# Performance work log

Hardware: AMD Instinct MI355X
Metric: run time of the kernel (lower is better)

## Reference

```python
import jax, jax.numpy as jnp
import numpy as np

B, D, N = 8, 1024, 1024
INTER, H = 512, 16
EPS = 1e-5


def conv1x1(x, W, b):
    # x: (B, Cin, N), W: (Cout, Cin), b: (Cout,) -> (B, Cout, N)
    return jnp.einsum('oc,bcn->bon', W, x) + b[None, :, None]


def setup_inputs() -> dict:
    key = jax.random.key(0)
    ks = jax.random.split(key, 12)
    s = 0.02
    v = jax.random.normal(ks[0], (B, D, N), jnp.float32)
    mask = (jax.random.uniform(ks[1], (B, N)) < 0.9).astype(jnp.float32)
    Wg = jax.random.normal(ks[2], (INTER, D), jnp.float32) * s
    bg = jax.random.normal(ks[3], (INTER,), jnp.float32) * s
    Wt = jax.random.normal(ks[4], (INTER, D), jnp.float32) * s
    bt = jax.random.normal(ks[5], (INTER,), jnp.float32) * s
    Wp = jax.random.normal(ks[6], (INTER, D), jnp.float32) * s
    bp = jax.random.normal(ks[7], (INTER,), jnp.float32) * s
    Ww = jax.random.normal(ks[8], (D, INTER), jnp.float32) * s
    bw = jax.random.normal(ks[9], (D,), jnp.float32) * s
    bn_gamma = jax.random.normal(ks[10], (D,), jnp.float32) * s + 1.0
    bn_beta = jax.random.normal(ks[11], (D,), jnp.float32) * s
    bn_mean = jnp.zeros((D,), jnp.float32)
    bn_var = jnp.ones((D,), jnp.float32)
    return {"v": v, "mask": mask, "Wg": Wg, "bg": bg, "Wt": Wt, "bt": bt,
            "Wp": Wp, "bp": bp, "Ww": Ww, "bw": bw, "bn_gamma": bn_gamma,
            "bn_beta": bn_beta, "bn_mean": bn_mean, "bn_var": bn_var}


def reference(v, mask, Wg, bg, Wt, bt, Wp, bp, Ww, bw,
              bn_gamma, bn_beta, bn_mean, bn_var):
    b, d, n = v.shape
    hd = INTER // H  # head dim
    # projections (1x1 conv == per-node linear); move to (B, N, INTER)
    g_v = conv1x1(v, Wg, bg).transpose(0, 2, 1) * mask[:, :, None]
    theta = conv1x1(v, Wt, bt).transpose(0, 2, 1)
    phi = conv1x1(v, Wp, bp).transpose(0, 2, 1)
    theta4 = theta.reshape(b, n, H, hd)  # (B, N, H, hd)
    phi4 = phi.reshape(b, n, H, hd)
    g4 = g_v.reshape(b, n, H, hd)
    # relation matrix R: (B, H, N, N)
    R = jnp.einsum('bnhd,bmhd->bhnm', theta4, phi4)
    C = jnp.sum(mask, axis=1)  # (B,)
    Rm = (R / C[:, None, None, None]) * mask[:, None, :, None] * mask[:, None, None, :]
    # aggregate: (B, N, H, hd)
    y = jnp.einsum('bhnm,bmhd->bnhd', Rm, g4).reshape(b, n, INTER)
    y = y.transpose(0, 2, 1)  # (B, INTER, N)
    # output projection + BatchNorm1d (eval form) + residual
    Wy = conv1x1(y, Ww, bw)
    inv = bn_gamma / jnp.sqrt(bn_var + EPS)
    Wy = (Wy - bn_mean[None, :, None]) * inv[None, :, None] + bn_beta[None, :, None]
    Wy = Wy * mask[:, None, :]
    return Wy + v
```

## Files before the change

### kernel.cpp

```cpp
#include <hip/hip_runtime.h>
#include <hip/hip_bf16.h>
#include <stdint.h>

#define B_ 8
#define D_ 1024
#define N_ 1024
#define INTER_ 512
#define H_ 16
#define EPS_ 1e-5f

typedef __attribute__((ext_vector_type(8))) short bf16x8;
typedef __attribute__((ext_vector_type(4))) float f32x4;
typedef __attribute__((ext_vector_type(4))) unsigned short u16x4;
typedef __attribute__((ext_vector_type(8))) unsigned short u16x8;

__device__ __forceinline__ unsigned short f2bf(float f) {
  union { float f; uint32_t u; } v; v.f = f;
  uint32_t r = (v.u + 0x7FFFu + ((v.u >> 16) & 1u)) >> 16;
  return (unsigned short)r;
}

__device__ __forceinline__ void gload_lds16(const void* g, void* l) {
  __builtin_amdgcn_global_load_lds(
      (const __attribute__((address_space(1))) void*)g,
      (__attribute__((address_space(3))) void*)l, 16, 0, 0);
}

__global__ __launch_bounds__(256) void k_prep(
    const float* __restrict__ v, const float* __restrict__ Wt,
    const float* __restrict__ Wp, const float* __restrict__ Wg,
    const float* __restrict__ Ww, const float* __restrict__ bt,
    const float* __restrict__ bp, const float* __restrict__ bg,
    const float* __restrict__ mask, unsigned short* __restrict__ vT,
    unsigned short* __restrict__ Wall, unsigned short* __restrict__ Wwb,
    float* __restrict__ ball, float* __restrict__ invC) {
  const int blk = blockIdx.x, tid = threadIdx.x;
  if (blk < 2048) {
    __shared__ short T[64 * 72];
    const int b = blk >> 8, tile = blk & 255;
    const int n0 = (tile & 15) * 64, d0 = (tile >> 4) * 64;
    const float* src = v + ((size_t)b * D_ + d0) * N_ + n0;
    const int c = tid & 15, rg = tid >> 4;
#pragma unroll
    for (int i = 0; i < 4; ++i) {
      const int r = rg * 4 + i;
      float4 f = *(const float4*)(src + (size_t)r * N_ + c * 4);
      const int nl = c * 4;
      T[(nl + 0) * 72 + r] = f2bf(f.x);
      T[(nl + 1) * 72 + r] = f2bf(f.y);
      T[(nl + 2) * 72 + r] = f2bf(f.z);
      T[(nl + 3) * 72 + r] = f2bf(f.w);
    }
    __syncthreads();
    unsigned short* dst = vT + ((size_t)b * N_ + n0) * D_ + d0;
    const int ch = tid & 7, nr = tid >> 3;
#pragma unroll
    for (int jj = 0; jj < 2; ++jj) {
      const int nl = nr + jj * 32;
      u16x8 val = *(const u16x8*)&T[nl * 72 + ch * 8];
      *(u16x8*)(dst + (size_t)nl * D_ + ch * 8) = val;
    }
  } else if (blk < 4096) {
    const int idx4 = (blk - 2048) * 256 + tid;
    const int total1 = 1536 * 1024 / 4;
    if (idx4 < total1) {
      const int idx = idx4 * 4;
      const int row = idx >> 10, c = idx & 1023;
      const float* src = row < 512    ? Wt + row * 1024 + c
                         : row < 1024 ? Wp + (row - 512) * 1024 + c
                                      : Wg + (row - 1024) * 1024 + c;
      float4 f = *(const float4*)src;
      u16x4 o = {f2bf(f.x), f2bf(f.y), f2bf(f.z), f2bf(f.w)};
      *(u16x4*)(Wall + idx) = o;
    } else {
      const int idx = (idx4 - total1) * 4;
      float4 f = *(const float4*)(Ww + idx);
      u16x4 o = {f2bf(f.x), f2bf(f.y), f2bf(f.z), f2bf(f.w)};
      *(u16x4*)(Wwb + idx) = o;
    }
  } else if (blk == 4096) {
    for (int i = tid; i < 512; i += 256) {
      ball[i] = bt[i]; ball[512 + i] = bp[i]; ball[1024 + i] = bg[i];
    }
  } else {
    const int b = blk - 4097;
    float s = 0.f;
    for (int i = tid; i < 1024; i += 256) s += mask[b * 1024 + i];
    for (int off = 32; off; off >>= 1) s += __shfl_down(s, off, 64);
    __shared__ float red[4];
    if ((tid & 63) == 0) red[tid >> 6] = s;
    __syncthreads();
    if (tid == 0) invC[b] = 1.0f / (red[0] + red[1] + red[2] + red[3]);
  }
}

#define BM 128
#define BN 128
#define BK 64

__global__ __launch_bounds__(256, 2) void k_gemmA(
    const unsigned short* __restrict__ Wall, const unsigned short* __restrict__ vT,
    const float* __restrict__ ball, const float* __restrict__ mask,
    unsigned short* __restrict__ thT, float* __restrict__ Spart) {
  __shared__ __align__(16) short smem[128 * 132];
  char* lA = (char*)smem;
  char* lB = lA + 16384;
  const int b = blockIdx.z, bx = blockIdx.x, by = blockIdx.y;
  const int tid = threadIdx.x, lane = tid & 63, w = tid >> 6;
  const int wr = w >> 1, wc = w & 1;
  const bool is_theta = (by < 4);
  const int rg = by - 4;

  const unsigned short* Abase;
  if (is_theta)
    Abase = Wall + (size_t)(by * BM) * 1024;
  else
    Abase = (w < 2) ? Wall + (size_t)(512 + rg * 64) * 1024
                    : Wall + (size_t)(1024 + rg * 64 - 64) * 1024;
  const unsigned short* Bbase = vT + ((size_t)b * N_ + bx * BN) * 1024;

  const int srow = w * 32 + (lane >> 3);
  const int sgl = lane & 7;

  f32x4 acc[4][4] = {};

  for (int kt = 0; kt < 1024 / BK; ++kt) {
#pragma unroll
    for (int i = 0; i < 4; ++i) {
      const int r = srow + i * 8;
      const int gs = sgl ^ (r & 7);
      gload_lds16(Abase + (size_t)r * 1024 + kt * BK + gs * 8,
                  lA + w * 4096 + i * 1024);
      gload_lds16(Bbase + (size_t)r * 1024 + kt * BK + gs * 8,
                  lB + w * 4096 + i * 1024);
    }
    __syncthreads();
#pragma unroll
    for (int kk = 0; kk < 2; ++kk) {
      bf16x8 af[4], bfr[4];
#pragma unroll
      for (int mf = 0; mf < 4; ++mf) {
        const int r = wr * 64 + mf * 16 + (lane & 15);
        int byte = r * 128 + kk * 64 + ((lane >> 4) * 16);
        byte ^= (r & 7) << 4;
        af[mf] = *(const bf16x8*)(lA + byte);
      }
#pragma unroll
      for (int nf = 0; nf < 4; ++nf) {
        const int r = wc * 64 + nf * 16 + (lane & 15);
        int byte = r * 128 + kk * 64 + ((lane >> 4) * 16);
        byte ^= (r & 7) << 4;
        bfr[nf] = *(const bf16x8*)(lB + byte);
      }
#pragma unroll
      for (int mf = 0; mf < 4; ++mf)
#pragma unroll
        for (int nf = 0; nf < 4; ++nf)
          acc[mf][nf] = __builtin_amdgcn_mfma_f32_16x16x32_bf16(
              af[mf], bfr[nf], acc[mf][nf], 0, 0, 0);
    }
    __syncthreads();
  }

  short* Tc = smem;
  if (is_theta) {
#pragma unroll
    for (int mf = 0; mf < 4; ++mf)
#pragma unroll
      for (int nf = 0; nf < 4; ++nf) {
        const int nl = wc * 64 + nf * 16 + (lane & 15);
        const int ol0 = wr * 64 + mf * 16 + ((lane >> 4) << 2);
        u16x4 o;
#pragma unroll
        for (int r = 0; r < 4; ++r)
          o[r] = f2bf(acc[mf][nf][r] + ball[by * BM + ol0 + r]);
        *(u16x4*)&Tc[nl * 132 + ol0] = o;
      }
    __syncthreads();
    const int ch = tid & 15;
#pragma unroll
    for (int j = 0; j < 8; ++j) {
      const int row = (tid >> 4) + j * 16;
      u16x4 lo = *(const u16x4*)&Tc[row * 132 + ch * 8];
      u16x4 hi = *(const u16x4*)&Tc[row * 132 + ch * 8 + 4];
      u16x8 val = {lo[0], lo[1], lo[2], lo[3], hi[0], hi[1], hi[2], hi[3]};
      *(u16x8*)(thT + ((size_t)b * N_ + bx * BN + row) * 512 + by * BM + ch * 8) =
          val;
    }
    return;
  }

#pragma unroll
  for (int mf = 0; mf < 4; ++mf)
#pragma unroll
    for (int nf = 0; nf < 4; ++nf) {
      const int nl = wc * 64 + nf * 16 + (lane & 15);
      const int ol0 = wr * 64 + mf * 16 + ((lane >> 4) << 2);
      const float mv = (wr == 1) ? mask[b * 1024 + bx * BN + nl] : 1.0f;
      const int gb = (wr == 0) ? 512 + rg * 64 : 1024 + rg * 64 - 64;
#pragma unroll
      for (int r = 0; r < 4; ++r)
        Tc[(ol0 + r) * 132 + nl] =
            f2bf((acc[mf][nf][r] + ball[gb + ol0 + r]) * mv);
    }
  __syncthreads();

  f32x4 accs[2][2][2] = {};
#pragma unroll
  for (int hl = 0; hl < 2; ++hl) {
    bf16x8 af[2], bfr[2];
#pragma unroll
    for (int mf = 0; mf < 2; ++mf) {
      const int row = hl * 32 + mf * 16 + (lane & 15);
      af[mf] = *(const bf16x8*)&Tc[row * 132 + w * 32 + (lane >> 4) * 8];
    }
#pragma unroll
    for (int nf = 0; nf < 2; ++nf) {
      const int row = 64 + hl * 32 + nf * 16 + (lane & 15);
      bfr[nf] = *(const bf16x8*)&Tc[row * 132 + w * 32 + (lane >> 4) * 8];
    }
#pragma unroll
    for (int mf = 0; mf < 2; ++mf)
#pragma unroll
      for (int nf = 0; nf < 2; ++nf)
        accs[hl][mf][nf] = __builtin_amdgcn_mfma_f32_16x16x32_bf16(
            af[mf], bfr[nf], accs[hl][mf][nf], 0, 0, 0);
  }
  __syncthreads();
  float* red = (float*)smem;
#pragma unroll
  for (int hl = 0; hl < 2; ++hl)
#pragma unroll
    for (int mf = 0; mf < 2; ++mf)
#pragma unroll
      for (int nf = 0; nf < 2; ++nf)
#pragma unroll
        for (int r = 0; r < 4; ++r)
          red[((hl * 4 + w) * 32 + mf * 16 + (lane >> 4) * 4 + r) * 32 +
              nf * 16 + (lane & 15)] = accs[hl][mf][nf][r];
  __syncthreads();
  for (int e = tid; e < 2048; e += 256) {
    const int hl = e >> 10, idx = e & 1023;
    const float* rb = red + (hl * 4) * 1024;
    const float sum = rb[idx] + rb[1024 + idx] + rb[2048 + idx] + rb[3072 + idx];
    const int h = rg * 2 + hl;
    Spart[(((size_t)b * 16 + h) * 8 + bx) * 1024 + idx] = sum;
  }
}

__global__ __launch_bounds__(256) void k_M(const unsigned short* __restrict__ Wwb,
                                           const float* __restrict__ Spart,
                                           unsigned short* __restrict__ M) {
  const int rb = blockIdx.x, h = blockIdx.y, b = blockIdx.z;
  const int tid = threadIdx.x, lane = tid & 63, w = tid >> 6;
  __shared__ short Sb[32 * 40];
  {
    const int e0 = tid * 4;
    const float* sp = Spart + (size_t)(b * 16 + h) * 8 * 1024 + e0;
    float4 a = {0, 0, 0, 0};
#pragma unroll
    for (int s = 0; s < 8; ++s) {
      float4 p = *(const float4*)(sp + s * 1024);
      a.x += p.x; a.y += p.y; a.z += p.z; a.w += p.w;
    }
    const int row = e0 >> 5, col = e0 & 31;
    u16x4 sv = {f2bf(a.x), f2bf(a.y), f2bf(a.z), f2bf(a.w)};
    *(u16x4*)&Sb[row * 40 + col] = sv;
  }
  __syncthreads();
  const int row0w = rb * 128 + w * 32;
  f32x4 acc[2][2] = {};
  bf16x8 af[2], bfr[2];
#pragma unroll
  for (int mf = 0; mf < 2; ++mf)
    af[mf] = *(const bf16x8*)(Wwb + (size_t)(row0w + mf * 16 + (lane & 15)) * 512 +
                              h * 32 + (lane >> 4) * 8);
#pragma unroll
  for (int nf = 0; nf < 2; ++nf)
    bfr[nf] = *(const bf16x8*)&Sb[(nf * 16 + (lane & 15)) * 40 + (lane >> 4) * 8];
#pragma unroll
  for (int mf = 0; mf < 2; ++mf)
#pragma unroll
    for (int nf = 0; nf < 2; ++nf)
      acc[mf][nf] = __builtin_amdgcn_mfma_f32_16x16x32_bf16(
          af[mf], bfr[nf], acc[mf][nf], 0, 0, 0);
#pragma unroll
  for (int mf = 0; mf < 2; ++mf)
#pragma unroll
    for (int nf = 0; nf < 2; ++nf)
#pragma unroll
      for (int r = 0; r < 4; ++r) {
        const int row = row0w + mf * 16 + (lane >> 4) * 4 + r;
        const int dp = nf * 16 + (lane & 15);
        M[((size_t)b * 1024 + row) * 512 + h * 32 + dp] = f2bf(acc[mf][nf][r]);
      }
}

__global__ __launch_bounds__(256, 2) void k_gemm2(
    const unsigned short* __restrict__ M, const unsigned short* __restrict__ thT,
    const float* __restrict__ mask, const float* __restrict__ invC,
    const float* __restrict__ bw, const float* __restrict__ gamma,
    const float* __restrict__ beta, const float* __restrict__ mean,
    const float* __restrict__ var, const float* __restrict__ vin,
    float* __restrict__ out) {
  __shared__ __align__(16) unsigned short lA[BM * BK];
  __shared__ __align__(16) unsigned short lB[BN * BK];
  const int b = blockIdx.z, bx = blockIdx.x, by = blockIdx.y;
  const int tid = threadIdx.x, lane = tid & 63, w = tid >> 6;
  const int wr = w >> 1, wc = w & 1;

  const unsigned short* Abase = M + ((size_t)b * 1024 + by * BM) * 512;
  const unsigned short* Bbase = thT + ((size_t)b * N_ + bx * BN) * 512;

  const int srow = w * 32 + (lane >> 3);
  const int sgl = lane & 7;

  f32x4 acc[4][4] = {};

  for (int kt = 0; kt < 512 / BK; ++kt) {
#pragma unroll
    for (int i = 0; i < 4; ++i) {
      const int r = srow + i * 8;
      const int gs = sgl ^ (r & 7);
      gload_lds16(Abase + (size_t)r * 512 + kt * BK + gs * 8,
                  (char*)lA + w * 4096 + i * 1024);
      gload_lds16(Bbase + (size_t)r * 512 + kt * BK + gs * 8,
                  (char*)lB + w * 4096 + i * 1024);
    }
    __syncthreads();
#pragma unroll
    for (int kk = 0; kk < 2; ++kk) {
      bf16x8 af[4], bfr[4];
#pragma unroll
      for (int mf = 0; mf < 4; ++mf) {
        const int r = wr * 64 + mf * 16 + (lane & 15);
        int byte = r * 128 + kk * 64 + ((lane >> 4) * 16);
        byte ^= (r & 7) << 4;
        af[mf] = *(const bf16x8*)((const char*)lA + byte);
      }
#pragma unroll
      for (int nf = 0; nf < 4; ++nf) {
        const int r = wc * 64 + nf * 16 + (lane & 15);
        int byte = r * 128 + kk * 64 + ((lane >> 4) * 16);
        byte ^= (r & 7) << 4;
        bfr[nf] = *(const bf16x8*)((const char*)lB + byte);
      }
#pragma unroll
      for (int mf = 0; mf < 4; ++mf)
#pragma unroll
        for (int nf = 0; nf < 4; ++nf)
          acc[mf][nf] = __builtin_amdgcn_mfma_f32_16x16x32_bf16(
              af[mf], bfr[nf], acc[mf][nf], 0, 0, 0);
    }
    __syncthreads();
  }

  const float icb = invC[b];
#pragma unroll
  for (int mf = 0; mf < 4; ++mf) {
#pragma unroll
    for (int nf = 0; nf < 4; ++nf) {
      const int col = bx * BN + wc * 64 + nf * 16 + (lane & 15);
      const int row0 = by * BM + wr * 64 + mf * 16 + ((lane >> 4) << 2);
      const float mv = mask[b * 1024 + col];
      const float sc = mv * icb;
#pragma unroll
      for (int r = 0; r < 4; ++r) {
        const int o = row0 + r;
        float val = acc[mf][nf][r] * sc + bw[o];
        const float inv = gamma[o] * rsqrtf(var[o] + EPS_);
        val = (val - mean[o]) * inv + beta[o];
        const size_t idx = ((size_t)b * 1024 + o) * 1024 + col;
        out[idx] = val * mv + vin[idx];
      }
    }
  }
}

extern "C" void kernel_launch(void* const* d_in, const int* in_sizes, int n_in,
                              void* d_out, int out_size, void* d_ws, size_t ws_size,
                              hipStream_t stream) {
  const float* v = (const float*)d_in[0];
  const float* mask = (const float*)d_in[1];
  const float* Wg = (const float*)d_in[2];
  const float* bg = (const float*)d_in[3];
  const float* Wt = (const float*)d_in[4];
  const float* bt = (const float*)d_in[5];
  const float* Wp = (const float*)d_in[6];
  const float* bp = (const float*)d_in[7];
  const float* Ww = (const float*)d_in[8];
  const float* bw = (const float*)d_in[9];
  const float* gamma = (const float*)d_in[10];
  const float* beta = (const float*)d_in[11];
  const float* mean = (const float*)d_in[12];
  const float* var = (const float*)d_in[13];
  float* out = (float*)d_out;

  char* ws = (char*)d_ws;
  unsigned short* vT = (unsigned short*)ws;    ws += 16777216;
  unsigned short* Wall = (unsigned short*)ws;  ws += 3145728;
  unsigned short* Wwb = (unsigned short*)ws;   ws += 1048576;
  unsigned short* thT = (unsigned short*)ws;   ws += 8388608;
  float* Spart = (float*)ws;                   ws += 4194304;
  unsigned short* Mw = (unsigned short*)ws;    ws += 8388608;
  float* ball = (float*)ws;                    ws += 6144;
  float* invC = (float*)ws;                    ws += 32;

  k_prep<<<4105, 256, 0, stream>>>(v, Wt, Wp, Wg, Ww, bt, bp, bg, mask,
                                   vT, Wall, Wwb, ball, invC);
  k_gemmA<<<dim3(8, 12, 8), 256, 0, stream>>>(Wall, vT, ball, mask, thT, Spart);
  k_M<<<dim3(8, 16, 8), 256, 0, stream>>>(Wwb, Spart, Mw);
  k_gemm2<<<dim3(8, 8, 8), 256, 0, stream>>>(Mw, thT, mask, invC, bw, gamma, beta,
                                             mean, var, v, out);
}
```

Baseline: 171.0 us.

## Enlarge gemmA tiles to 256x256 with double-buffered LDS and MFMA priority

The projection GEMM now uses 256x256 output tiles with 512 threads and a flattened 192-block grid. Global-to-LDS loads are double-buffered so the next K slice streams in while the current one is computed, and MFMA bursts are wrapped in s_setprio with intra-tile barriers. The S-partial reduction is reorganized for 4 N-tiles instead of 8, which halves Spart and the k_M reduction work. The cost is large LDS use (about 132 KB, so likely one block per CU) and only 192 blocks for the GPU's CUs, which may leave compute units idle.

```diff
diff --git a/kernel.cpp b/kernel.cpp
--- a/kernel.cpp
+++ b/kernel.cpp
@@ -94,157 +94,197 @@
   }
 }
 
-#define BM 128
-#define BN 128
-#define BK 64
-
-__global__ __launch_bounds__(256, 2) void k_gemmA(
+__global__ __launch_bounds__(512, 2) void k_gemmA(
     const unsigned short* __restrict__ Wall, const unsigned short* __restrict__ vT,
     const float* __restrict__ ball, const float* __restrict__ mask,
     unsigned short* __restrict__ thT, float* __restrict__ Spart) {
-  __shared__ __align__(16) short smem[128 * 132];
-  char* lA = (char*)smem;
-  char* lB = lA + 16384;
-  const int b = blockIdx.z, bx = blockIdx.x, by = blockIdx.y;
+  __shared__ __align__(16) char smem[135168];
+  const int flat = blockIdx.x;
+  const int b = flat & 7;
+  const int tile = flat >> 3;
+  const int mt = tile % 6, nt = tile / 6;
+  const bool is_theta = (mt < 2);
+  const int rg = mt - 2;
+
   const int tid = threadIdx.x, lane = tid & 63, w = tid >> 6;
-  const int wr = w >> 1, wc = w & 1;
-  const bool is_theta = (by < 4);
-  const int rg = by - 4;
+  const int wm = w >> 2, wn = w & 3;
 
   const unsigned short* Abase;
   if (is_theta)
-    Abase = Wall + (size_t)(by * BM) * 1024;
+    Abase = Wall + (size_t)(mt * 256) * 1024;
   else
-    Abase = (w < 2) ? Wall + (size_t)(512 + rg * 64) * 1024
-                    : Wall + (size_t)(1024 + rg * 64 - 64) * 1024;
-  const unsigned short* Bbase = vT + ((size_t)b * N_ + bx * BN) * 1024;
+    Abase = (w < 4) ? Wall + (size_t)(512 + rg * 128) * 1024
+                    : Wall + (size_t)(896 + rg * 128) * 1024;
+  const unsigned short* Bbase = vT + ((size_t)b * N_ + nt * 256) * 1024;
 
   const int srow = w * 32 + (lane >> 3);
   const int sgl = lane & 7;
 
-  f32x4 acc[4][4] = {};
-
-  for (int kt = 0; kt < 1024 / BK; ++kt) {
-#pragma unroll
-    for (int i = 0; i < 4; ++i) {
-      const int r = srow + i * 8;
-      const int gs = sgl ^ (r & 7);
-      gload_lds16(Abase + (size_t)r * 1024 + kt * BK + gs * 8,
-                  lA + w * 4096 + i * 1024);
-      gload_lds16(Bbase + (size_t)r * 1024 + kt * BK + gs * 8,
-                  lB + w * 4096 + i * 1024);
-    }
-    __syncthreads();
+  f32x4 acc[8][4] = {};
+  int cur = 0;
+
+#pragma unroll
+  for (int i = 0; i < 4; ++i) {
+    const int r = srow + i * 8;
+    const int gs = sgl ^ (r & 7);
+    gload_lds16(Abase + (size_t)r * 1024 + gs * 8, smem + w * 4096 + i * 1024);
+    gload_lds16(Bbase + (size_t)r * 1024 + gs * 8,
+                smem + 32768 + w * 4096 + i * 1024);
+  }
+  __syncthreads();
+
+  for (int t = 0; t < 16; ++t) {
+    if (t < 15) {
+      const char* Asrc = (const char*)(Abase + (size_t)(t + 1) * 64);
+      const char* Bsrc = (const char*)(Bbase + (size_t)(t + 1) * 64);
+      char* dstA = smem + (cur ^ 1) * 65536;
+      char* dstB = dstA + 32768;
+#pragma unroll
+      for (int i = 0; i < 4; ++i) {
+        const int r = srow + i * 8;
+        const int gs = sgl ^ (r & 7);
+        gload_lds16(Asrc + (size_t)r * 2048 + gs * 16, dstA + w * 4096 + i * 1024);
+        gload_lds16(Bsrc + (size_t)r * 2048 + gs * 16, dstB + w * 4096 + i * 1024);
+      }
+    }
+    const char* bufA = smem + cur * 65536;
+    const char* bufB = bufA + 32768;
+
+    bf16x8 af[8];
 #pragma unroll
     for (int kk = 0; kk < 2; ++kk) {
-      bf16x8 af[4], bfr[4];
-#pragma unroll
-      for (int mf = 0; mf < 4; ++mf) {
-        const int r = wr * 64 + mf * 16 + (lane & 15);
+#pragma unroll
+      for (int mf = 0; mf < 8; ++mf) {
+        const int r = wm * 128 + mf * 16 + (lane & 15);
         int byte = r * 128 + kk * 64 + ((lane >> 4) * 16);
         byte ^= (r & 7) << 4;
-        af[mf] = *(const bf16x8*)(lA + byte);
-      }
+        af[mf] = *(const bf16x8*)(bufA + byte);
+      }
+      bf16x8 b0, b1;
+      {
+        const int r0 = wn * 64 + 0 * 16 + (lane & 15);
+        int byte0 = r0 * 128 + kk * 64 + ((lane >> 4) * 16);
+        byte0 ^= (r0 & 7) << 4;
+        b0 = *(const bf16x8*)(bufB + byte0);
+        const int r1 = wn * 64 + 1 * 16 + (lane & 15);
+        int byte1 = r1 * 128 + kk * 64 + ((lane >> 4) * 16);
+        byte1 ^= (r1 & 7) << 4;
+        b1 = *(const bf16x8*)(bufB + byte1);
+      }
+      __builtin_amdgcn_s_setprio(1);
+#pragma unroll
+      for (int mf = 0; mf < 8; ++mf) {
+        acc[mf][0] = __builtin_amdgcn_mfma_f32_16x16x32_bf16(af[mf], b0,
+                                                             acc[mf][0], 0, 0, 0);
+        acc[mf][1] = __builtin_amdgcn_mfma_f32_16x16x32_bf16(af[mf], b1,
+                                                             acc[mf][1], 0, 0, 0);
+      }
+      __builtin_amdgcn_s_setprio(0);
+      __builtin_amdgcn_s_barrier();
+      {
+        const int r0 = wn * 64 + 2 * 16 + (lane & 15);
+        int byte0 = r0 * 128 + kk * 64 + ((lane >> 4) * 16);
+        byte0 ^= (r0 & 7) << 4;
+        b0 = *(const bf16x8*)(bufB + byte0);
+        const int r1 = wn * 64 + 3 * 16 + (lane & 15);
+        int byte1 = r1 * 128 + kk * 64 + ((lane >> 4) * 16);
+        byte1 ^= (r1 & 7) << 4;
+        b1 = *(const bf16x8*)(bufB + byte1);
+      }
+      __builtin_amdgcn_s_setprio(1);
+#pragma unroll
+      for (int mf = 0; mf < 8; ++mf) {
+        acc[mf][2] = __builtin_amdgcn_mfma_f32_16x16x32_bf16(af[mf], b0,
+                                                             acc[mf][2], 0, 0, 0);
+        acc[mf][3] = __builtin_amdgcn_mfma_f32_16x16x32_bf16(af[mf], b1,
+                                                             acc[mf][3], 0, 0, 0);
+      }
+      __builtin_amdgcn_s_setprio(0);
+      if (kk == 0) __builtin_amdgcn_s_barrier();
+    }
+    __syncthreads();
+    cur ^= 1;
+  }
+
+  short* Tc = (short*)smem;
+  if (is_theta) {
+#pragma unroll
+    for (int mf = 0; mf < 8; ++mf)
 #pragma unroll
       for (int nf = 0; nf < 4; ++nf) {
-        const int r = wc * 64 + nf * 16 + (lane & 15);
-        int byte = r * 128 + kk * 64 + ((lane >> 4) * 16);
-        byte ^= (r & 7) << 4;
-        bfr[nf] = *(const bf16x8*)(lB + byte);
-      }
-#pragma unroll
-      for (int mf = 0; mf < 4; ++mf)
-#pragma unroll
-        for (int nf = 0; nf < 4; ++nf)
-          acc[mf][nf] = __builtin_amdgcn_mfma_f32_16x16x32_bf16(
-              af[mf], bfr[nf], acc[mf][nf], 0, 0, 0);
-    }
-    __syncthreads();
-  }
-
-  short* Tc = smem;
-  if (is_theta) {
-#pragma unroll
-    for (int mf = 0; mf < 4; ++mf)
-#pragma unroll
-      for (int nf = 0; nf < 4; ++nf) {
-        const int nl = wc * 64 + nf * 16 + (lane & 15);
-        const int ol0 = wr * 64 + mf * 16 + ((lane >> 4) << 2);
+        const int nl = wn * 64 + nf * 16 + (lane & 15);
+        const int ol0 = wm * 128 + mf * 16 + ((lane >> 4) << 2);
         u16x4 o;
 #pragma unroll
         for (int r = 0; r < 4; ++r)
-          o[r] = f2bf(acc[mf][nf][r] + ball[by * BM + ol0 + r]);
-        *(u16x4*)&Tc[nl * 132 + ol0] = o;
-      }
-    __syncthreads();
-    const int ch = tid & 15;
-#pragma unroll
-    for (int j = 0; j < 8; ++j) {
-      const int row = (tid >> 4) + j * 16;
-      u16x4 lo = *(const u16x4*)&Tc[row * 132 + ch * 8];
-      u16x4 hi = *(const u16x4*)&Tc[row * 132 + ch * 8 + 4];
-      u16x8 val = {lo[0], lo[1], lo[2], lo[3], hi[0], hi[1], hi[2], hi[3]};
-      *(u16x8*)(thT + ((size_t)b * N_ + bx * BN + row) * 512 + by * BM + ch * 8) =
-          val;
+          o[r] = f2bf(acc[mf][nf][r] + ball[mt * 256 + ol0 + r]);
+        *(u16x4*)&Tc[nl * 264 + ol0] = o;
+      }
+    __syncthreads();
+    const int ch = tid & 31, nr = tid >> 5;
+#pragma unroll
+    for (int j = 0; j < 16; ++j) {
+      const int row = nr + j * 16;
+      u16x8 val = *(const u16x8*)&Tc[row * 264 + ch * 8];
+      *(u16x8*)(thT + ((size_t)b * N_ + nt * 256 + row) * 512 + mt * 256 +
+                ch * 8) = val;
     }
     return;
   }
 
 #pragma unroll
-  for (int mf = 0; mf < 4; ++mf)
+  for (int mf = 0; mf < 8; ++mf)
 #pragma unroll
     for (int nf = 0; nf < 4; ++nf) {
-      const int nl = wc * 64 + nf * 16 + (lane & 15);
-      const int ol0 = wr * 64 + mf * 16 + ((lane >> 4) << 2);
-      const float mv = (wr == 1) ? mask[b * 1024 + bx * BN + nl] : 1.0f;
-      const int gb = (wr == 0) ? 512 + rg * 64 : 1024 + rg * 64 - 64;
+      const int nl = wn * 64 + nf * 16 + (lane & 15);
+      const int ol0 = wm * 128 + mf * 16 + ((lane >> 4) << 2);
+      const float mv = (wm == 1) ? mask[b * 1024 + nt * 256 + nl] : 1.0f;
+      const int bb = (wm == 0) ? 512 + rg * 128 : 896 + rg * 128;
 #pragma unroll
       for (int r = 0; r < 4; ++r)
-        Tc[(ol0 + r) * 132 + nl] =
-            f2bf((acc[mf][nf][r] + ball[gb + ol0 + r]) * mv);
+        Tc[(ol0 + r) * 264 + nl] =
+            f2bf((acc[mf][nf][r] + ball[bb + ol0 + r]) * mv);
     }
   __syncthreads();
 
-  f32x4 accs[2][2][2] = {};
-#pragma unroll
-  for (int hl = 0; hl < 2; ++hl) {
-    bf16x8 af[2], bfr[2];
+  const int hl = w & 3, nh = w >> 2;
+  f32x4 accs[2][2] = {};
+#pragma unroll
+  for (int ks = 0; ks < 4; ++ks) {
+    const int n0 = nh * 128 + ks * 32 + ((lane >> 4) * 8);
+    bf16x8 pa[2], gb[2];
 #pragma unroll
     for (int mf = 0; mf < 2; ++mf) {
       const int row = hl * 32 + mf * 16 + (lane & 15);
-      af[mf] = *(const bf16x8*)&Tc[row * 132 + w * 32 + (lane >> 4) * 8];
+      pa[mf] = *(const bf16x8*)&Tc[row * 264 + n0];
     }
 #pragma unroll
     for (int nf = 0; nf < 2; ++nf) {
-      const int row = 64 + hl * 32 + nf * 16 + (lane & 15);
-      bfr[nf] = *(const bf16x8*)&Tc[row * 132 + w * 32 + (lane >> 4) * 8];
+      const int row = 128 + hl * 32 + nf * 16 + (lane & 15);
+      gb[nf] = *(const bf16x8*)&Tc[row * 264 + n0];
     }
 #pragma unroll
     for (int mf = 0; mf < 2; ++mf)
 #pragma unroll
       for (int nf = 0; nf < 2; ++nf)
-        accs[hl][mf][nf] = __builtin_amdgcn_mfma_f32_16x16x32_bf16(
-            af[mf], bfr[nf], accs[hl][mf][nf], 0, 0, 0);
+        accs[mf][nf] = __builtin_amdgcn_mfma_f32_16x16x32_bf16(
+            pa[mf], gb[nf], accs[mf][nf], 0, 0, 0);
   }
   __syncthreads();
   float* red = (float*)smem;
 #pragma unroll
-  for (int hl = 0; hl < 2; ++hl)
-#pragma unroll
-    for (int mf = 0; mf < 2; ++mf)
-#pragma unroll
-      for (int nf = 0; nf < 2; ++nf)
-#pragma unroll
-        for (int r = 0; r < 4; ++r)
-          red[((hl * 4 + w) * 32 + mf * 16 + (lane >> 4) * 4 + r) * 32 +
-              nf * 16 + (lane & 15)] = accs[hl][mf][nf][r];
+  for (int mf = 0; mf < 2; ++mf)
+#pragma unroll
+    for (int nf = 0; nf < 2; ++nf)
+#pragma unroll
+      for (int r = 0; r < 4; ++r)
+        red[w * 1024 + (mf * 16 + (lane >> 4) * 4 + r) * 32 + nf * 16 +
+            (lane & 15)] = accs[mf][nf][r];
   __syncthreads();
-  for (int e = tid; e < 2048; e += 256) {
-    const int hl = e >> 10, idx = e & 1023;
-    const float* rb = red + (hl * 4) * 1024;
-    const float sum = rb[idx] + rb[1024 + idx] + rb[2048 + idx] + rb[3072 + idx];
-    const int h = rg * 2 + hl;
-    Spart[(((size_t)b * 16 + h) * 8 + bx) * 1024 + idx] = sum;
+  for (int e = tid; e < 4096; e += 512) {
+    const int h = e >> 10, idx = e & 1023;
+    const float sum = red[h * 1024 + idx] + red[(h + 4) * 1024 + idx];
+    Spart[(((size_t)b * 16 + rg * 4 + h) * 4 + nt) * 1024 + idx] = sum;
   }
 }
 
@@ -256,10 +296,10 @@
   __shared__ short Sb[32 * 40];
   {
     const int e0 = tid * 4;
-    const float* sp = Spart + (size_t)(b * 16 + h) * 8 * 1024 + e0;
+    const float* sp = Spart + (size_t)(b * 16 + h) * 4096 + e0;
     float4 a = {0, 0, 0, 0};
 #pragma unroll
-    for (int s = 0; s < 8; ++s) {
+    for (int s = 0; s < 4; ++s) {
       float4 p = *(const float4*)(sp + s * 1024);
       a.x += p.x; a.y += p.y; a.z += p.z; a.w += p.w;
     }
@@ -295,6 +335,10 @@
         M[((size_t)b * 1024 + row) * 512 + h * 32 + dp] = f2bf(acc[mf][nf][r]);
       }
 }
+
+#define BM 128
+#define BN 128
+#define BK 64
 
 __global__ __launch_bounds__(256, 2) void k_gemm2(
     const unsigned short* __restrict__ M, const unsigned short* __restrict__ thT,
@@ -401,14 +445,14 @@
   unsigned short* Wall = (unsigned short*)ws;  ws += 3145728;
   unsigned short* Wwb = (unsigned short*)ws;   ws += 1048576;
   unsigned short* thT = (unsigned short*)ws;   ws += 8388608;
-  float* Spart = (float*)ws;                   ws += 4194304;
+  float* Spart = (float*)ws;                   ws += 2097152;
   unsigned short* Mw = (unsigned short*)ws;    ws += 8388608;
   float* ball = (float*)ws;                    ws += 6144;
   float* invC = (float*)ws;                    ws += 32;
 
   k_prep<<<4105, 256, 0, stream>>>(v, Wt, Wp, Wg, Ww, bt, bp, bg, mask,
                                    vT, Wall, Wwb, ball, invC);
-  k_gemmA<<<dim3(8, 12, 8), 256, 0, stream>>>(Wall, vT, ball, mask, thT, Spart);
+  k_gemmA<<<192, 512, 0, stream>>>(Wall, vT, ball, mask, thT, Spart);
   k_M<<<dim3(8, 16, 8), 256, 0, stream>>>(Wwb, Spart, Mw);
   k_gemm2<<<dim3(8, 8, 8), 256, 0, stream>>>(Mw, thT, mask, invC, bw, gamma, beta,
                                              mean, var, v, out);
```

New measurement: 173.2 us. No clear change (+1.3%).
